# Kernel tuning notes

Hardware: AMD Instinct MI355X
Metric: run time of the kernel (lower is better)

Reference implementation:

```python
import jax, jax.numpy as jnp
import numpy as np

B, T, IN, H, L, OUT = 128, 1024, 256, 512, 2, 256


def setup_inputs() -> dict:
    key = jax.random.key(0)
    ks = jax.random.split(key, 12)
    s_in = 1.0 / np.sqrt(H)  # torch RNNCell init scale (uniform +-1/sqrt(H))
    u = lambda k, shape: jax.random.uniform(k, shape, jnp.float32, -s_in, s_in)
    return {
        "x": jax.random.normal(ks[0], (B, T, IN), jnp.float32),
        "h0": jnp.zeros((L, B, H), jnp.float32),
        "w_ih0": u(ks[1], (H, IN)),
        "w_hh0": u(ks[2], (H, H)),
        "b_ih0": u(ks[3], (H,)),
        "b_hh0": u(ks[4], (H,)),
        "w_ih1": u(ks[5], (H, H)),
        "w_hh1": u(ks[6], (H, H)),
        "b_ih1": u(ks[7], (H,)),
        "b_hh1": u(ks[8], (H,)),
        "fc_w": u(ks[9], (OUT, H)),
        "fc_b": u(ks[10], (OUT,)),
    }


def reference(x, h0, w_ih0, w_hh0, b_ih0, b_hh0, w_ih1, w_hh1, b_ih1, b_hh1, fc_w, fc_b):
    # x: [B, T, IN] -> scan over time axis
    xt = jnp.swapaxes(x, 0, 1)  # [T, B, IN]

    def step(hs, x_t):
        h0_, h1_ = hs
        h0n = jnp.tanh(x_t @ w_ih0.T + b_ih0 + h0_ @ w_hh0.T + b_hh0)
        h1n = jnp.tanh(h0n @ w_ih1.T + b_ih1 + h1_ @ w_hh1.T + b_hh1)
        return (h0n, h1n), None

    (h0f, h1f), _ = jax.lax.scan(step, (h0[0], h0[1]), xt)
    # original: out = outs[-1].squeeze(); fc(out). squeeze is a no-op for B>1.
    return h1f @ fc_w.T + fc_b
```

## Files before the change

kernel.cpp:

```cpp
#include <hip/hip_runtime.h>

#define BB   128
#define TT   1024
#define INP  256
#define HH   512
#define OUTD 256
#define GB   16
#define NG   8
#define NBLK 256

typedef float  f32x4  __attribute__((ext_vector_type(4)));
typedef short  short8 __attribute__((ext_vector_type(8)));
typedef unsigned long long u64;

__device__ __forceinline__ unsigned short bf16_rne(float f) {
  union { float f; unsigned u; } v; v.f = f;
  unsigned r = v.u + 0x7fffu + ((v.u >> 16) & 1u);
  return (unsigned short)(r >> 16);
}

__device__ __forceinline__ float fast_tanh(float x) {
  float t = __builtin_amdgcn_exp2f(x * 2.8853900817779268f);
  return 1.0f - 2.0f * __builtin_amdgcn_rcpf(t + 1.0f);
}

__device__ __forceinline__ short8 pack8(f32x4 a, f32x4 b) {
  union { unsigned short s[8]; short8 v; } u;
  u.s[0] = bf16_rne(a[0]); u.s[1] = bf16_rne(a[1]);
  u.s[2] = bf16_rne(a[2]); u.s[3] = bf16_rne(a[3]);
  u.s[4] = bf16_rne(b[0]); u.s[5] = bf16_rne(b[1]);
  u.s[6] = bf16_rne(b[2]); u.s[7] = bf16_rne(b[3]);
  return u.v;
}

__device__ __forceinline__ short8 load_cvt8(const float* p) {
  const f32x4* q = (const f32x4*)p;
  return pack8(q[0], q[1]);
}

__device__ __forceinline__ f32x4 ntload4(const float* p) {
  return __builtin_nontemporal_load((const f32x4*)p);
}

__device__ __forceinline__ short8 l2load8(const unsigned short* p) {
  union { u64 q[2]; short8 v; } u;
  const u64* pp = (const u64*)p;
  u.q[0] = __hip_atomic_load(pp,     __ATOMIC_RELAXED, __HIP_MEMORY_SCOPE_AGENT);
  u.q[1] = __hip_atomic_load(pp + 1, __ATOMIC_RELAXED, __HIP_MEMORY_SCOPE_AGENT);
  return u.v;
}

__device__ __forceinline__ unsigned short* hslot(unsigned short* base, int slot, int g) {
  return base + ((size_t)(slot * NG + g)) * (16 * 64 * 8);
}

__global__ void __launch_bounds__(256, 1) rnn_mfma(
    const float* __restrict__ x,
    const float* __restrict__ h0init,
    const float* __restrict__ w_ih0,
    const float* __restrict__ w_hh0,
    const float* __restrict__ b_ih0,
    const float* __restrict__ b_hh0,
    const float* __restrict__ w_ih1,
    const float* __restrict__ w_hh1,
    const float* __restrict__ b_ih1,
    const float* __restrict__ b_hh1,
    const float* __restrict__ fc_w,
    const float* __restrict__ fc_b,
    float* __restrict__ out,
    unsigned* __restrict__ ws_ctl,
    unsigned short* __restrict__ h0f,
    unsigned short* __restrict__ h1f)
{
  extern __shared__ char lds_pad[];
  (void)lds_pad;
  const int tid = threadIdx.x;

  __shared__ unsigned sh_tk, sh_g;
  if (tid == 0) {
    unsigned xcc;
    asm volatile("s_getreg_b32 %0, hwreg(HW_REG_XCC_ID)" : "=s"(xcc));
    xcc &= 7;
    sh_g  = xcc;
    sh_tk = __hip_atomic_fetch_add(ws_ctl + xcc * 32, 1u,
                                   __ATOMIC_RELAXED, __HIP_MEMORY_SCOPE_AGENT);
  }
  __syncthreads();
  const unsigned ticket = sh_tk;
  const int g = (int)sh_g;
  if (ticket >= 16) return;

  const int role = (int)ticket;
  const bool isL0 = role < 8;
  const int wv   = tid >> 6;
  const int lane = tid & 63;
  const int ln   = lane & 15;
  const int q    = lane >> 4;
  const int j0   = (role & 7) * 64 + wv * 16 + ln;
  const int jq   = (role & 7) * 64 + wv * 16 + q * 4;
  const int bg   = g * GB;

  volatile int* flags  = (volatile int*)(ws_ctl + 1024 + g * 512);
  volatile int* myflag = flags + role * 32;

  for (int c = tid; c < 2048; c += 256) {
    int a  = c >> 10;
    int bl = (c >> 6) & 15;
    int j8 = (c & 63) * 8;
    short8 v = load_cvt8(h0init + ((size_t)a * BB + (bg + bl)) * HH + j8);
    unsigned short* dst = hslot(a ? h1f : h0f, 3, g)
        + ((size_t)((j8 >> 5) * 64 + ((j8 >> 3) & 3) * 16 + bl)) * 8;
    *(short8*)dst = v;
  }
  __syncthreads();
  if (tid == 0) *myflag = 1;

  short8 Bf0[24];
  short8 Bf1[32];
  if (isL0) {
#pragma unroll
    for (int kb = 0; kb < 24; ++kb) {
      int k = kb * 32 + q * 8;
      const float* src = (k < INP) ? (w_ih0 + (size_t)j0 * INP + k)
                                   : (w_hh0 + (size_t)j0 * HH + (k - INP));
      Bf0[kb] = load_cvt8(src);
    }
  } else {
#pragma unroll
    for (int kb = 0; kb < 32; ++kb) {
      int k = kb * 32 + q * 8;
      const float* src = (k < HH) ? (w_ih1 + (size_t)j0 * HH + k)
                                  : (w_hh1 + (size_t)j0 * HH + (k - HH));
      Bf1[kb] = load_cvt8(src);
    }
  }
  f32x4 bias4;
  {
    const float* bi = isL0 ? b_ih0 : b_ih1;
    const float* bh = isL0 ? b_hh0 : b_hh1;
    bias4 = *(const f32x4*)(bi + jq) + *(const f32x4*)(bh + jq);
  }

  short8 xa[8];
  if (isL0) {
    const float* xp = x + ((size_t)(bg + ln) * TT + 0) * INP;
#pragma unroll
    for (int kb = 0; kb < 8; ++kb)
      xa[kb] = pack8(ntload4(xp + kb * 32 + q * 8), ntload4(xp + kb * 32 + q * 8 + 4));
  }

  const f32x4 z = {0.f, 0.f, 0.f, 0.f};
  const int tmax = isL0 ? (TT - 1) : TT;

#pragma unroll 1
  for (int t = 0; t <= tmax; ++t) {
    if (isL0) {
      f32x4 xr[16];
      const bool havex = (t + 1 < TT);
      if (havex) {
        const float* xp = x + ((size_t)(bg + ln) * TT + (t + 1)) * INP;
#pragma unroll
        for (int kb = 0; kb < 8; ++kb) {
          xr[2 * kb]     = ntload4(xp + kb * 32 + q * 8);
          xr[2 * kb + 1] = ntload4(xp + kb * 32 + q * 8 + 4);
        }
      }

      if (tid < 16) {
        volatile int* fp = flags + tid * 32;
        const int thr = (tid < 8) ? (t + 1) : (t - 1);
        while (*fp < thr) {}
      }
      __syncthreads();

      const unsigned short* hp0 = hslot(h0f, (t + 3) & 3, g);
      short8 Af[16];
#pragma unroll
      for (int kb = 0; kb < 16; ++kb)
        Af[kb] = l2load8(hp0 + ((size_t)kb * 64 + lane) * 8);

      f32x4 ac[4] = {z, z, z, z};
#pragma unroll
      for (int kb = 0; kb < 8; ++kb)
        ac[kb & 3] = __builtin_amdgcn_mfma_f32_16x16x32_bf16(
            Bf0[kb], xa[kb], ac[kb & 3], 0, 0, 0);
#pragma unroll
      for (int kb = 8; kb < 24; ++kb)
        ac[kb & 3] = __builtin_amdgcn_mfma_f32_16x16x32_bf16(
            Bf0[kb], Af[kb - 8], ac[kb & 3], 0, 0, 0);

      f32x4 d = ac[0] + ac[1] + ac[2] + ac[3];
      unsigned short* wdst = hslot(h0f, t & 3, g);
      union { unsigned short s[4]; u64 q8; } uu;
#pragma unroll
      for (int r = 0; r < 4; ++r)
        uu.s[r] = bf16_rne(fast_tanh(d[r] + bias4[r]));
      *(u64*)(wdst + (size_t)((jq >> 5) * 64 + ((jq >> 3) & 3) * 16 + ln) * 8
              + (jq & 7)) = uu.q8;
      if (havex) {
#pragma unroll
        for (int kb = 0; kb < 8; ++kb)
          xa[kb] = pack8(xr[2 * kb], xr[2 * kb + 1]);
      }
    } else {
      if (tid >= 8 && tid < 16) {
        volatile int* fp = flags + tid * 32;
        while (*fp < t + 1) {}
      }
      __syncthreads();

      const unsigned short* hp1 = hslot(h1f, (t + 2) & 3, g);
      short8 Af1[16];
#pragma unroll
      for (int kb = 0; kb < 16; ++kb)
        Af1[kb] = l2load8(hp1 + ((size_t)kb * 64 + lane) * 8);

      if (tid < 8) {
        volatile int* fp = flags + tid * 32;
        while (*fp < t + 1) {}
      }
      __syncthreads();

      if (t >= 1) {
        const unsigned short* hp0 = hslot(h0f, (t + 3) & 3, g);
        short8 Af0[16];
#pragma unroll
        for (int kb = 0; kb < 16; ++kb)
          Af0[kb] = l2load8(hp0 + ((size_t)kb * 64 + lane) * 8);

        f32x4 ac[4] = {z, z, z, z};
#pragma unroll
        for (int kb = 0; kb < 16; ++kb)
          ac[kb & 3] = __builtin_amdgcn_mfma_f32_16x16x32_bf16(
              Bf1[kb + 16], Af1[kb], ac[kb & 3], 0, 0, 0);
#pragma unroll
        for (int kb = 0; kb < 16; ++kb)
          ac[kb & 3] = __builtin_amdgcn_mfma_f32_16x16x32_bf16(
              Bf1[kb], Af0[kb], ac[kb & 3], 0, 0, 0);

        f32x4 d = ac[0] + ac[1] + ac[2] + ac[3];
        unsigned short* wdst = hslot(h1f, (t + 3) & 3, g);
        union { unsigned short s[4]; u64 q8; } uu;
#pragma unroll
        for (int r = 0; r < 4; ++r)
          uu.s[r] = bf16_rne(fast_tanh(d[r] + bias4[r]));
        *(u64*)(wdst + (size_t)((jq >> 5) * 64 + ((jq >> 3) & 3) * 16 + ln) * 8
                + (jq & 7)) = uu.q8;
      }
    }

    __syncthreads();
    if (tid == 0) *myflag = t + 2;
  }

  if (tid < 16) {
    volatile int* fp = flags + tid * 32;
    const int thr = (tid < 8) ? (TT + 1) : (TT + 2);
    while (*fp < thr) {}
  }
  __syncthreads();

  if (wv == 0) {
    const unsigned short* hp = hslot(h1f, 3, g);
    const int o_ln = role * 16 + ln;
    const int o_q  = role * 16 + q * 4;
    f32x4 ac[4] = {z, z, z, z};
#pragma unroll
    for (int kb = 0; kb < 16; ++kb) {
      int k = kb * 32 + q * 8;
      short8 Bfc = load_cvt8(fc_w + (size_t)o_ln * HH + k);
      short8 Af  = l2load8(hp + ((size_t)kb * 64 + lane) * 8);
      ac[kb & 3] = __builtin_amdgcn_mfma_f32_16x16x32_bf16(
          Bfc, Af, ac[kb & 3], 0, 0, 0);
    }
    f32x4 fb = *(const f32x4*)(fc_b + o_q);
    f32x4 v = ac[0] + ac[1] + ac[2] + ac[3] + fb;
    *(f32x4*)(out + (size_t)(bg + ln) * OUTD + o_q) = v;
  }
}

extern "C" void kernel_launch(void* const* d_in, const int* in_sizes, int n_in,
                              void* d_out, int out_size, void* d_ws, size_t ws_size,
                              hipStream_t stream) {
  (void)in_sizes; (void)n_in; (void)out_size; (void)ws_size;

  const float* x      = (const float*)d_in[0];
  const float* h0init = (const float*)d_in[1];
  const float* w_ih0  = (const float*)d_in[2];
  const float* w_hh0  = (const float*)d_in[3];
  const float* b_ih0  = (const float*)d_in[4];
  const float* b_hh0  = (const float*)d_in[5];
  const float* w_ih1  = (const float*)d_in[6];
  const float* w_hh1  = (const float*)d_in[7];
  const float* b_ih1  = (const float*)d_in[8];
  const float* b_hh1  = (const float*)d_in[9];
  const float* fc_w   = (const float*)d_in[10];
  const float* fc_b   = (const float*)d_in[11];
  float* out = (float*)d_out;

  unsigned* ws_ctl = (unsigned*)d_ws;
  unsigned short* h0f = (unsigned short*)((char*)d_ws + 32768);
  unsigned short* h1f = h0f + 4 * NG * (16 * 64 * 8);

  hipMemsetAsync(d_ws, 0, 32768, stream);

  rnn_mfma<<<dim3(NBLK), dim3(256), 90112, stream>>>(
      x, h0init, w_ih0, w_hh0, b_ih0, b_hh0, w_ih1, w_hh1, b_ih1, b_hh1,
      fc_w, fc_b, out, ws_ctl, h0f, h1f);
}
```

Baseline: 4.153 ms.

## Offload layer-0 input projection to producer blocks running ahead of recurrence

Adds four producer workgroups per XCC group that compute x_t @ w_ih0^T with MFMA up to two steps ahead and publish fp32 results to a 4-slot ring buffer in workspace, signalled by flags. Layer-0 recurrence blocks no longer load and convert x or run the 8 input MFMAs. They wait on the producer flags, read the precomputed projection and add it before tanh. This shortens the serial critical path per timestep. The cost is extra flag polling, more workspace traffic and more active blocks per group.

```diff
diff --git a/kernel.cpp b/kernel.cpp
--- a/kernel.cpp
+++ b/kernel.cpp
@@ -44,6 +44,14 @@
 
 __device__ __forceinline__ short8 l2load8(const unsigned short* p) {
   union { u64 q[2]; short8 v; } u;
+  const u64* pp = (const u64*)p;
+  u.q[0] = __hip_atomic_load(pp,     __ATOMIC_RELAXED, __HIP_MEMORY_SCOPE_AGENT);
+  u.q[1] = __hip_atomic_load(pp + 1, __ATOMIC_RELAXED, __HIP_MEMORY_SCOPE_AGENT);
+  return u.v;
+}
+
+__device__ __forceinline__ f32x4 l2load4f(const float* p) {
+  union { u64 q[2]; f32x4 v; } u;
   const u64* pp = (const u64*)p;
   u.q[0] = __hip_atomic_load(pp,     __ATOMIC_RELAXED, __HIP_MEMORY_SCOPE_AGENT);
   u.q[1] = __hip_atomic_load(pp + 1, __ATOMIC_RELAXED, __HIP_MEMORY_SCOPE_AGENT);
@@ -70,7 +78,8 @@
     float* __restrict__ out,
     unsigned* __restrict__ ws_ctl,
     unsigned short* __restrict__ h0f,
-    unsigned short* __restrict__ h1f)
+    unsigned short* __restrict__ h1f,
+    float* __restrict__ u0r)
 {
   extern __shared__ char lds_pad[];
   (void)lds_pad;
@@ -88,19 +97,67 @@
   __syncthreads();
   const unsigned ticket = sh_tk;
   const int g = (int)sh_g;
-  if (ticket >= 16) return;
-
-  const int role = (int)ticket;
-  const bool isL0 = role < 8;
+  if (ticket >= 20) return;
+
   const int wv   = tid >> 6;
   const int lane = tid & 63;
   const int ln   = lane & 15;
   const int q    = lane >> 4;
+  const int bg   = g * GB;
+  volatile int* flags = (volatile int*)(ws_ctl + 1024 + g * 1024);
+  const f32x4 z = {0.f, 0.f, 0.f, 0.f};
+
+  if (ticket >= 16) {
+    const int prod = (int)ticket - 16;
+    short8 Wp[16];
+#pragma unroll
+    for (int jt = 0; jt < 2; ++jt)
+#pragma unroll
+      for (int kb = 0; kb < 8; ++kb)
+        Wp[jt * 8 + kb] = load_cvt8(
+            w_ih0 + (size_t)(prod * 128 + wv * 32 + jt * 16 + ln) * INP
+            + kb * 32 + q * 8);
+    volatile int* pf = flags + (16 + prod) * 32;
+
+#pragma unroll 1
+    for (int t = 0; t < TT; ++t) {
+      if (tid < 8) {
+        volatile int* fp = flags + tid * 32;
+        const int thr = t - 2;
+        while (*fp < thr) __builtin_amdgcn_s_sleep(1);
+      }
+      __syncthreads();
+
+      short8 xa[8];
+      const float* xp = x + ((size_t)(bg + ln) * TT + t) * INP;
+#pragma unroll
+      for (int kb = 0; kb < 8; ++kb)
+        xa[kb] = pack8(ntload4(xp + kb * 32 + q * 8),
+                       ntload4(xp + kb * 32 + q * 8 + 4));
+
+      f32x4 acc[2] = {z, z};
+#pragma unroll
+      for (int jt = 0; jt < 2; ++jt)
+#pragma unroll
+        for (int kb = 0; kb < 8; ++kb)
+          acc[jt] = __builtin_amdgcn_mfma_f32_16x16x32_bf16(
+              Wp[jt * 8 + kb], xa[kb], acc[jt], 0, 0, 0);
+
+      float* slotbase = u0r + ((size_t)((t & 3) * NG + g)) * 8192;
+#pragma unroll
+      for (int jt = 0; jt < 2; ++jt)
+        *(f32x4*)(slotbase
+            + ((size_t)((prod * 32 + wv * 8 + jt * 4 + q) * 16 + ln)) * 4) = acc[jt];
+      __syncthreads();
+      if (tid == 0) *pf = t + 2;
+    }
+    return;
+  }
+
+  const int role = (int)ticket;
+  const bool isL0 = role < 8;
   const int j0   = (role & 7) * 64 + wv * 16 + ln;
   const int jq   = (role & 7) * 64 + wv * 16 + q * 4;
-  const int bg   = g * GB;
-
-  volatile int* flags  = (volatile int*)(ws_ctl + 1024 + g * 512);
   volatile int* myflag = flags + role * 32;
 
   for (int c = tid; c < 2048; c += 256) {
@@ -115,16 +172,12 @@
   __syncthreads();
   if (tid == 0) *myflag = 1;
 
-  short8 Bf0[24];
+  short8 Bf0[16];
   short8 Bf1[32];
   if (isL0) {
 #pragma unroll
-    for (int kb = 0; kb < 24; ++kb) {
-      int k = kb * 32 + q * 8;
-      const float* src = (k < INP) ? (w_ih0 + (size_t)j0 * INP + k)
-                                   : (w_hh0 + (size_t)j0 * HH + (k - INP));
-      Bf0[kb] = load_cvt8(src);
-    }
+    for (int kb = 0; kb < 16; ++kb)
+      Bf0[kb] = load_cvt8(w_hh0 + (size_t)j0 * HH + kb * 32 + q * 8);
   } else {
 #pragma unroll
     for (int kb = 0; kb < 32; ++kb) {
@@ -141,35 +194,18 @@
     bias4 = *(const f32x4*)(bi + jq) + *(const f32x4*)(bh + jq);
   }
 
-  short8 xa[8];
-  if (isL0) {
-    const float* xp = x + ((size_t)(bg + ln) * TT + 0) * INP;
-#pragma unroll
-    for (int kb = 0; kb < 8; ++kb)
-      xa[kb] = pack8(ntload4(xp + kb * 32 + q * 8), ntload4(xp + kb * 32 + q * 8 + 4));
-  }
-
-  const f32x4 z = {0.f, 0.f, 0.f, 0.f};
   const int tmax = isL0 ? (TT - 1) : TT;
 
 #pragma unroll 1
   for (int t = 0; t <= tmax; ++t) {
     if (isL0) {
-      f32x4 xr[16];
-      const bool havex = (t + 1 < TT);
-      if (havex) {
-        const float* xp = x + ((size_t)(bg + ln) * TT + (t + 1)) * INP;
-#pragma unroll
-        for (int kb = 0; kb < 8; ++kb) {
-          xr[2 * kb]     = ntload4(xp + kb * 32 + q * 8);
-          xr[2 * kb + 1] = ntload4(xp + kb * 32 + q * 8 + 4);
-        }
-      }
-
       if (tid < 16) {
         volatile int* fp = flags + tid * 32;
         const int thr = (tid < 8) ? (t + 1) : (t - 1);
         while (*fp < thr) {}
+      } else if (tid < 20) {
+        volatile int* fp = flags + tid * 32;
+        while (*fp < t + 2) {}
       }
       __syncthreads();
 
@@ -178,18 +214,17 @@
 #pragma unroll
       for (int kb = 0; kb < 16; ++kb)
         Af[kb] = l2load8(hp0 + ((size_t)kb * 64 + lane) * 8);
+      const float* up = u0r + ((size_t)((t & 3) * NG + g)) * 8192
+          + ((size_t)((((role & 7) * 16 + wv * 4 + q) * 16) + ln)) * 4;
+      f32x4 u0v = l2load4f(up);
 
       f32x4 ac[4] = {z, z, z, z};
 #pragma unroll
-      for (int kb = 0; kb < 8; ++kb)
+      for (int kb = 0; kb < 16; ++kb)
         ac[kb & 3] = __builtin_amdgcn_mfma_f32_16x16x32_bf16(
-            Bf0[kb], xa[kb], ac[kb & 3], 0, 0, 0);
-#pragma unroll
-      for (int kb = 8; kb < 24; ++kb)
-        ac[kb & 3] = __builtin_amdgcn_mfma_f32_16x16x32_bf16(
-            Bf0[kb], Af[kb - 8], ac[kb & 3], 0, 0, 0);
-
-      f32x4 d = ac[0] + ac[1] + ac[2] + ac[3];
+            Bf0[kb], Af[kb], ac[kb & 3], 0, 0, 0);
+
+      f32x4 d = ac[0] + ac[1] + ac[2] + ac[3] + u0v;
       unsigned short* wdst = hslot(h0f, t & 3, g);
       union { unsigned short s[4]; u64 q8; } uu;
 #pragma unroll
@@ -197,18 +232,12 @@
         uu.s[r] = bf16_rne(fast_tanh(d[r] + bias4[r]));
       *(u64*)(wdst + (size_t)((jq >> 5) * 64 + ((jq >> 3) & 3) * 16 + ln) * 8
               + (jq & 7)) = uu.q8;
-      if (havex) {
-#pragma unroll
-        for (int kb = 0; kb < 8; ++kb)
-          xa[kb] = pack8(xr[2 * kb], xr[2 * kb + 1]);
-      }
     } else {
       if (tid >= 8 && tid < 16) {
         volatile int* fp = flags + tid * 32;
         while (*fp < t + 1) {}
       }
       __syncthreads();
-
       const unsigned short* hp1 = hslot(h1f, (t + 2) & 3, g);
       short8 Af1[16];
 #pragma unroll
@@ -299,12 +328,13 @@
   float* out = (float*)d_out;
 
   unsigned* ws_ctl = (unsigned*)d_ws;
-  unsigned short* h0f = (unsigned short*)((char*)d_ws + 32768);
+  unsigned short* h0f = (unsigned short*)((char*)d_ws + 65536);
   unsigned short* h1f = h0f + 4 * NG * (16 * 64 * 8);
-
-  hipMemsetAsync(d_ws, 0, 32768, stream);
+  float* u0r = (float*)((char*)d_ws + 65536 + 2 * 4 * NG * (16 * 64 * 8) * 2);
+
+  hipMemsetAsync(d_ws, 0, 65536, stream);
 
   rnn_mfma<<<dim3(NBLK), dim3(256), 90112, stream>>>(
       x, h0init, w_ih0, w_hh0, b_ih0, b_hh0, w_ih1, w_hh1, b_ih1, b_hh1,
-      fc_w, fc_b, out, ws_ctl, h0f, h1f);
-}
+      fc_w, fc_b, out, ws_ctl, h0f, h1f, u0r);
+}
```

Result: faster. 3.483 ms (-16.1%).
